# Performance work log

Measured on AMD Instinct MI355X. Metric: run time of the kernel, lower is better.

Reference implementation:

```python
import jax, jax.numpy as jnp
import numpy as np

N_NODES = 10000
N_EDGES = 160000
HIDDEN = 128
NGAUSS = 100
NF = 64
N_CONV = 2


def setup_inputs() -> dict:
    key = jax.random.key(0)
    ks = jax.random.split(key, 10)
    h = jax.random.normal(ks[0], (N_NODES, HIDDEN), dtype=jnp.float32)
    edge_index = jax.random.randint(ks[1], (2, N_EDGES), 0, N_NODES, dtype=jnp.int64)
    edge_weight = jax.random.uniform(ks[2], (N_EDGES,), dtype=jnp.float32)
    edge_attr = jax.random.normal(ks[3], (N_EDGES, NGAUSS), dtype=jnp.float32)
    data = jnp.zeros((1,), dtype=jnp.float32)
    s = 0.05
    lin0_w = jax.random.normal(ks[4], (HIDDEN, NF), dtype=jnp.float32) * s
    lin0_b = jnp.zeros((NF,), dtype=jnp.float32)
    nn_w1 = jax.random.normal(ks[5], (NGAUSS, HIDDEN), dtype=jnp.float32) * s
    nn_b1 = jnp.zeros((HIDDEN,), dtype=jnp.float32)
    nn_w2 = jax.random.normal(ks[6], (HIDDEN, NF * NF), dtype=jnp.float32) * s
    nn_b2 = jnp.zeros((NF * NF,), dtype=jnp.float32)
    root_w = jax.random.normal(ks[7], (NF, NF), dtype=jnp.float32) * s
    conv_b = jnp.zeros((NF,), dtype=jnp.float32)
    return {"h": h, "edge_index": edge_index, "edge_weight": edge_weight,
            "edge_attr": edge_attr, "data": data,
            "lin0_w": lin0_w, "lin0_b": lin0_b,
            "nn_w1": nn_w1, "nn_b1": nn_b1, "nn_w2": nn_w2, "nn_b2": nn_b2,
            "root_w": root_w, "conv_b": conv_b}


def reference(h, edge_index, edge_weight, edge_attr, data,
              lin0_w, lin0_b, nn_w1, nn_b1, nn_w2, nn_b2, root_w, conv_b):
    # lin0 + relu -> node features x: [N, nf]
    x = jax.nn.relu(h @ lin0_w + lin0_b)

    # edge network: per-edge weight matrix W_e: [E, nf, nf]
    hidden = jax.nn.relu(edge_attr @ nn_w1 + nn_b1)
    W_e = (hidden @ nn_w2 + nn_b2).reshape(N_EDGES, NF, NF)

    src = edge_index[0]  # message source (x_j)
    dst = edge_index[1]  # aggregation target (i)

    # in-degree for mean aggregation (0-degree nodes -> 0 output)
    deg = jax.ops.segment_sum(jnp.ones((N_EDGES,), x.dtype), dst, num_segments=N_NODES)
    inv_deg = (1.0 / jnp.maximum(deg, 1.0))[:, None]  # [N, 1]

    # n_conv applications of the SAME NNConv (shared weights)
    for _ in range(N_CONV):
        msg = jnp.einsum('ei,eio->eo', x[src], W_e)  # gather + per-edge matvec
        agg = jax.ops.segment_sum(msg, dst, num_segments=N_NODES) * inv_deg
        x = agg + x @ root_w + conv_b
    return x
```

## Files before the change

### kernel.cpp

```cpp
#include <hip/hip_runtime.h>

#define N_NODES 10000
#define N_EDGES 160000
#define HID 128
#define NG 100
#define NF 64
#define NIO 4096
#define NJ 8192
#define M_PAD 10240

#define PREP_LIN0 2500
#define PREP_WPT (PREP_LIN0 + 2112)

typedef short bf16x8 __attribute__((ext_vector_type(8)));
typedef float f32x4 __attribute__((ext_vector_type(4)));

__device__ __forceinline__ unsigned short f2b(float f) {
    unsigned int u = __float_as_uint(f);
    u += 0x7fffu + ((u >> 16) & 1u);
    return (unsigned short)(u >> 16);
}
__device__ __forceinline__ float b2f(unsigned short s) { return __uint_as_float((unsigned int)s << 16); }

__device__ __forceinline__ long fidx64(int row, int k) {
    return (long)(row >> 4) * 1024 + (k >> 5) * 512 + ((((k >> 3) & 3) * 16 + (row & 15))) * 8 + (k & 7);
}
__device__ __forceinline__ long fidx128(int row, int k) {
    return (long)(row >> 4) * 2048 + (k >> 5) * 512 + ((((k >> 3) & 3) * 16 + (row & 15))) * 8 + (k & 7);
}

__global__ void hist_kernel(const int* __restrict__ src, const int* __restrict__ dst,
                            float* __restrict__ deg, int* __restrict__ cnt) {
    int e = blockIdx.x * 256 + threadIdx.x;
    if (e < N_EDGES) {
        atomicAdd(&deg[dst[e]], 1.0f);
        atomicAdd(&cnt[src[e]], 1);
    }
}

#define SCAN_C 40
__global__ void scan_kernel(const int* __restrict__ cnt, const float* __restrict__ deg,
                            int* __restrict__ rowptr, float* __restrict__ invd) {
    __shared__ int wsum[4];
    int t = threadIdx.x, wv = t >> 6, l = t & 63;
    int base_i = t * SCAN_C;
    int loc[SCAN_C];
    int sum = 0;
#pragma unroll
    for (int j = 0; j < SCAN_C; ++j) {
        int g = base_i + j;
        int v = (g < N_NODES) ? cnt[g] : 0;
        loc[j] = sum;
        sum += v;
    }
    int incl = sum;
    for (int off = 1; off < 64; off <<= 1) {
        int v = __shfl_up(incl, off);
        if (l >= off) incl += v;
    }
    if (l == 63) wsum[wv] = incl;
    __syncthreads();
    int wbase = 0;
#pragma unroll
    for (int w = 0; w < 4; ++w) wbase += (w < wv) ? wsum[w] : 0;
    int tbase = wbase + incl - sum;
#pragma unroll
    for (int j = 0; j < SCAN_C; ++j) {
        int g = base_i + j;
        if (g <= N_NODES) rowptr[g] = tbase + loc[j];
        if (g < N_NODES) invd[g] = 1.0f / fmaxf(deg[g], 1.0f);
    }
}

__global__ void scatter_kernel(const int* __restrict__ src, const int* __restrict__ dst,
                               const int* __restrict__ rowptr, int* __restrict__ fill,
                               int* __restrict__ rankOf, int* __restrict__ dstp) {
    int e = blockIdx.x * 256 + threadIdx.x;
    if (e < N_EDGES) {
        int s = src[e];
        int r = rowptr[s] + atomicAdd(&fill[s], 1);
        rankOf[e] = r;
        dstp[r] = dst[e];
    }
}

__global__ void prep_kernel(const float* __restrict__ h, const float* __restrict__ lw,
                            const float* __restrict__ lb, const float* __restrict__ b2,
                            float* __restrict__ x, unsigned short* __restrict__ xh,
                            float* __restrict__ xb2,
                            const float* __restrict__ w1, const float* __restrict__ w2,
                            unsigned short* __restrict__ w1h, unsigned short* __restrict__ w2h) {
    int bid = blockIdx.x;
    if (bid < PREP_LIN0) {
        int wv = threadIdx.x >> 6, l = threadIdx.x & 63;
        int n = bid * 4 + wv;
        float h0 = h[n * HID + l];
        float h1 = h[n * HID + 64 + l];
        float acc = lb[l];
#pragma unroll
        for (int i = 0; i < 64; ++i) {
            acc += __shfl(h0, i) * lw[i * NF + l];
            acc += __shfl(h1, i) * lw[(64 + i) * NF + l];
        }
        float v = fmaxf(acc, 0.0f);
        x[n * NF + l] = v;
        xh[fidx64(n, l)] = f2b(v);
        float xb = 0.0f;
#pragma unroll
        for (int i = 0; i < 64; ++i) xb += __shfl(v, i) * b2[i * 64 + l];
        xb2[n * NF + l] = xb;
    } else {
        int id = (bid - PREP_LIN0) * 256 + threadIdx.x;
        if (id < HID * HID) {
            int k = id & 127, c = id >> 7;
            float v = (k < NG) ? w1[k * HID + c] : 0.0f;
            w1h[fidx128(c, k)] = f2b(v);
        } else {
            int id2 = id - HID * HID;
            int i = id2 & 63, j = id2 >> 6;
            int o = j >> 7, k = j & 127;
            w2h[fidx64(j, i)] = f2b(w2[k * NIO + i * 64 + o]);
        }
    }
}

__launch_bounds__(256)
__global__ void hgemm_kernel(const float* __restrict__ ea, const int* __restrict__ rankOf,
                             const unsigned short* __restrict__ w1h,
                             const float* __restrict__ b1, unsigned short* __restrict__ hidp) {
    __shared__ float stg[4][1056];
    const int tid = threadIdx.x, wv = tid >> 6, l = tid & 63;
    const long grow = (long)blockIdx.x * 128;
    const int wr = (wv >> 1) * 64, wc = (wv & 1) * 64;
    const long bpan0 = (wc >> 4);
    const int lc = l & 15, lk = l >> 4;
    const int r8 = l >> 3, cg = l & 7;

    int rks[4][2];
#pragma unroll
    for (int m = 0; m < 4; ++m)
#pragma unroll
        for (int it = 0; it < 2; ++it)
            rks[m][it] = rankOf[grow + wr + m * 16 + it * 8 + r8];

    f32x4 acc[4][4] = {};
#pragma unroll
    for (int ks = 0; ks < 4; ++ks) {
        const int c0 = ks * 32 + lk * 8;
        bf16x8 a[4], b[4];
#pragma unroll
        for (int m = 0; m < 4; ++m) {
            const float* Ar = ea + (grow + wr + m * 16 + lc) * (long)NG;
            f32x4 lo = {0.0f, 0.0f, 0.0f, 0.0f}, hi = {0.0f, 0.0f, 0.0f, 0.0f};
            if (c0 <= 88) {
                lo = *(const f32x4*)(Ar + c0);
                hi = *(const f32x4*)(Ar + c0 + 4);
            } else if (c0 == 96) {
                lo = *(const f32x4*)(Ar + 96);
            }
            bf16x8 t;
            t[0] = f2b(lo[0]); t[1] = f2b(lo[1]); t[2] = f2b(lo[2]); t[3] = f2b(lo[3]);
            t[4] = f2b(hi[0]); t[5] = f2b(hi[1]); t[6] = f2b(hi[2]); t[7] = f2b(hi[3]);
            a[m] = t;
        }
#pragma unroll
        for (int n = 0; n < 4; ++n)
            b[n] = *(const bf16x8*)(w1h + (bpan0 + n) * 2048 + ks * 512 + (long)l * 8);
#pragma unroll
        for (int m = 0; m < 4; ++m)
#pragma unroll
            for (int n = 0; n < 4; ++n)
                acc[m][n] = __builtin_amdgcn_mfma_f32_16x16x32_bf16(a[m], b[n], acc[m][n], 0, 0, 0);
    }

    float* s = stg[wv];
#pragma unroll
    for (int m = 0; m < 4; ++m) {
#pragma unroll
        for (int n = 0; n < 4; ++n)
#pragma unroll
            for (int q = 0; q < 4; ++q)
                s[((l >> 4) * 4 + q) * 66 + n * 16 + (l & 15)] = acc[m][n][q];
#pragma unroll
        for (int it = 0; it < 2; ++it) {
            int row = it * 8 + r8;
            const float* sr = s + row * 66 + cg * 8;
            int colbase = wc + cg * 8;
            unsigned int u[4];
#pragma unroll
            for (int p = 0; p < 4; ++p) {
                float f0 = fmaxf(sr[2 * p] + b1[colbase + 2 * p], 0.0f);
                float f1 = fmaxf(sr[2 * p + 1] + b1[colbase + 2 * p + 1], 0.0f);
                u[p] = ((unsigned int)f2b(f1) << 16) | f2b(f0);
            }
            long Ro = rks[m][it];
            *(uint4*)(hidp + Ro * HID + colbase) = make_uint4(u[0], u[1], u[2], u[3]);
        }
    }
}

__launch_bounds__(256)
__global__ void ygemm_kernel(const unsigned short* __restrict__ xh,
                             const unsigned short* __restrict__ wh,
                             unsigned short* __restrict__ y, int n0) {
    __shared__ float stg[4][1056];
    const int tid = threadIdx.x, wv = tid >> 6, l = tid & 63;
    const int grow = blockIdx.x * 128;
    const int col0base = blockIdx.y * 256;
    const int wr = (wv >> 1) * 64, wc = (wv & 1) * 64;
    const long apan0 = ((n0 + grow + wr) >> 4);
    const int r8 = l >> 3, cg = l & 7;

    bf16x8 a[2][4];
#pragma unroll
    for (int ks = 0; ks < 2; ++ks)
#pragma unroll
        for (int m = 0; m < 4; ++m)
            a[ks][m] = *(const bf16x8*)(xh + (apan0 + m) * 1024 + ks * 512 + (long)l * 8);

    for (int ct = 0; ct < 2; ++ct) {
        const int col0 = col0base + ct * 128;
        const long bpan0 = ((col0 + wc) >> 4);
        f32x4 acc[4][4] = {};
#pragma unroll
        for (int ks = 0; ks < 2; ++ks) {
            bf16x8 b[4];
#pragma unroll
            for (int n = 0; n < 4; ++n)
                b[n] = *(const bf16x8*)(wh + (bpan0 + n) * 1024 + ks * 512 + (long)l * 8);
#pragma unroll
            for (int m = 0; m < 4; ++m)
#pragma unroll
                for (int n = 0; n < 4; ++n)
                    acc[m][n] = __builtin_amdgcn_mfma_f32_16x16x32_bf16(a[ks][m], b[n], acc[m][n], 0, 0, 0);
        }

        float* s = stg[wv];
#pragma unroll
        for (int m = 0; m < 4; ++m) {
#pragma unroll
            for (int n = 0; n < 4; ++n)
#pragma unroll
                for (int q = 0; q < 4; ++q)
                    s[((l >> 4) * 4 + q) * 66 + n * 16 + (l & 15)] = acc[m][n][q];
#pragma unroll
            for (int it = 0; it < 2; ++it) {
                int row = it * 8 + r8;
                const float* sr = s + row * 66 + cg * 8;
                unsigned int u[4];
#pragma unroll
                for (int p = 0; p < 4; ++p)
                    u[p] = ((unsigned int)f2b(sr[2 * p + 1]) << 16) | f2b(sr[2 * p]);
                long R = grow + wr + m * 16 + row;
                *(uint4*)(y + R * NJ + col0 + wc + cg * 8) = make_uint4(u[0], u[1], u[2], u[3]);
            }
        }
    }
}

__global__ void matvec_mfma_kernel(const unsigned short* __restrict__ y,
                                   const unsigned short* __restrict__ hidp,
                                   const int* __restrict__ rowptr, const int* __restrict__ dstp,
                                   const float* __restrict__ xb2, float* __restrict__ agg,
                                   int n0, int n1) {
    int wv = threadIdx.x >> 6, l = threadIdx.x & 63;
    int s = n0 + blockIdx.x * 4 + wv;
    if (s >= n1) return;
    int r0 = rowptr[s], r1 = rowptr[s + 1];
    if (r0 == r1) return;
    int lc = l & 15, lk = l >> 4;

    const unsigned short* Ys = y + (long)(s - n0) * NJ;
    bf16x8 b[4][4];
    float xb2v[4];
#pragma unroll
    for (int og = 0; og < 4; ++og) {
        const unsigned short* Yo = Ys + (og * 16 + lc) * HID + lk * 8;
#pragma unroll
        for (int ks = 0; ks < 4; ++ks) b[og][ks] = *(const bf16x8*)(Yo + ks * 32);
        xb2v[og] = xb2[(long)s * NF + og * 16 + lc];
    }

    for (int mt = r0; mt < r1; mt += 16) {
        const unsigned short* Hs = hidp + (long)(mt + lc) * HID + lk * 8;
        bf16x8 a[4];
#pragma unroll
        for (int ks = 0; ks < 4; ++ks) a[ks] = *(const bf16x8*)(Hs + ks * 32);
        f32x4 acc[4] = {};
#pragma unroll
        for (int og = 0; og < 4; ++og)
#pragma unroll
            for (int ks = 0; ks < 4; ++ks)
                acc[og] = __builtin_amdgcn_mfma_f32_16x16x32_bf16(a[ks], b[og][ks], acc[og], 0, 0, 0);
#pragma unroll
        for (int q = 0; q < 4; ++q) {
            int rank = mt + lk * 4 + q;
            if (rank < r1) {
                long base = (long)dstp[rank] * NF;
#pragma unroll
                for (int og = 0; og < 4; ++og)
                    atomicAdd(&agg[base + og * 16 + lc], acc[og][q] + xb2v[og]);
            }
        }
    }
}

__global__ void combine_kernel(const float* __restrict__ x, float* __restrict__ agg,
                               const float* __restrict__ invd, const float* __restrict__ rw,
                               const float* __restrict__ cb, const float* __restrict__ b2,
                               float* __restrict__ xo, unsigned short* __restrict__ xh,
                               float* __restrict__ xb2) {
    int wv = threadIdx.x >> 6, l = threadIdx.x & 63;
    int n = blockIdx.x * 4 + wv;
    float xv = x[n * NF + l];
    float acc = cb[l];
#pragma unroll
    for (int i = 0; i < 64; ++i) acc += __shfl(xv, i) * rw[i * NF + l];
    float av = agg[n * NF + l];
    agg[n * NF + l] = 0.0f;
    float v = av * invd[n] + acc;
    xo[n * NF + l] = v;
    if (xh) {
        xh[fidx64(n, l)] = f2b(v);
        float xb = 0.0f;
#pragma unroll
        for (int i = 0; i < 64; ++i) xb += __shfl(v, i) * b2[i * 64 + l];
        xb2[n * NF + l] = xb;
    }
}

extern "C" void kernel_launch(void* const* d_in, const int* in_sizes, int n_in,
                              void* d_out, int out_size, void* d_ws, size_t ws_size,
                              hipStream_t stream) {
    const float* h = (const float*)d_in[0];
    const int* ei = (const int*)d_in[1];
    const float* ea = (const float*)d_in[3];
    const float* lin0_w = (const float*)d_in[5];
    const float* lin0_b = (const float*)d_in[6];
    const float* nn_w1 = (const float*)d_in[7];
    const float* nn_b1 = (const float*)d_in[8];
    const float* nn_w2 = (const float*)d_in[9];
    const float* nn_b2 = (const float*)d_in[10];
    const float* root_w = (const float*)d_in[11];
    const float* conv_b = (const float*)d_in[12];
    const int* srcIdx = ei;
    const int* dstIdx = ei + N_EDGES;

    const size_t fixed =
        (size_t)(N_EDGES + 16) * HID * 2 +
        (size_t)NJ * NF * 2 +
        (size_t)HID * HID * 2 +
        (size_t)M_PAD * NF * 2 +
        (size_t)N_NODES * NF * 4 * 4 +
        3 * 40192 +
        (size_t)N_NODES * 4 +
        (size_t)(N_NODES + 1) * 4 +
        (size_t)N_EDGES * 4 * 2 +
        32768;
    int nc = 0, CSn = 0;
    size_t region_bytes = 0;
    for (int c = 2; c <= 16; c *= 2) {
        int csn = (((N_NODES + c - 1) / c) + 127) & ~127;
        size_t rb = (size_t)csn * NJ * 2;
        if (fixed + rb <= ws_size) { nc = c; CSn = csn; region_bytes = rb; break; }
    }
    if (nc == 0) {
        hipMemsetAsync(d_out, 0, (size_t)out_size * 4, stream);
        return;
    }

    char* ws = (char*)d_ws;
    size_t off = 0;
    auto alloc = [&](size_t bytes) {
        char* p = ws + off;
        off += (bytes + 255) & ~(size_t)255;
        return p;
    };
    unsigned short* y = (unsigned short*)alloc(region_bytes);
    unsigned short* hidp = (unsigned short*)alloc((size_t)(N_EDGES + 16) * HID * 2);
    unsigned short* w2h = (unsigned short*)alloc((size_t)NJ * NF * 2);
    unsigned short* w1h = (unsigned short*)alloc((size_t)HID * HID * 2);
    unsigned short* xh = (unsigned short*)alloc((size_t)M_PAD * NF * 2);
    float* xA = (float*)alloc((size_t)N_NODES * NF * 4);
    float* xB = (float*)alloc((size_t)N_NODES * NF * 4);
    float* agg = (float*)alloc((size_t)N_NODES * NF * 4);
    float* xb2 = (float*)alloc((size_t)N_NODES * NF * 4);
    char* degblk = alloc(3 * 40192);
    float* deg = (float*)degblk;
    int* cnt = (int*)(degblk + 40192);
    int* fill = (int*)(degblk + 2 * 40192);
    float* invd = (float*)alloc((size_t)N_NODES * 4);
    int* rowptr = (int*)alloc((size_t)(N_NODES + 1) * 4);
    int* rankOf = (int*)alloc((size_t)N_EDGES * 4);
    int* dstp = (int*)alloc((size_t)N_EDGES * 4);

    hipMemsetAsync(degblk, 0, 3 * 40192, stream);
    hipMemsetAsync(agg, 0, (size_t)N_NODES * NF * 4, stream);
    hist_kernel<<<(N_EDGES + 255) / 256, 256, 0, stream>>>(srcIdx, dstIdx, deg, cnt);
    scan_kernel<<<1, 256, 0, stream>>>(cnt, deg, rowptr, invd);
    scatter_kernel<<<(N_EDGES + 255) / 256, 256, 0, stream>>>(srcIdx, dstIdx, rowptr, fill, rankOf, dstp);
    prep_kernel<<<PREP_WPT, 256, 0, stream>>>(h, lin0_w, lin0_b, nn_b2, xA, xh, xb2,
                                              nn_w1, nn_w2, w1h, w2h);
    hgemm_kernel<<<N_EDGES / 128, 256, 0, stream>>>(ea, rankOf, w1h, nn_b1, hidp);

    for (int conv = 0; conv < 2; ++conv) {
        const float* xin = conv ? xB : xA;
        float* xout = conv ? (float*)d_out : xB;
        unsigned short* mh = conv ? nullptr : xh;

        for (int c = 0; c < nc; ++c) {
            int n0 = c * CSn;
            int n1 = n0 + CSn; if (n1 > N_NODES) n1 = N_NODES;
            if (n0 >= N_NODES) break;
            int gx = (n1 - n0 + 127) / 128;
            ygemm_kernel<<<dim3(gx, NJ / 256), 256, 0, stream>>>(xh, w2h, y, n0);
            matvec_mfma_kernel<<<(n1 - n0 + 3) / 4, 256, 0, stream>>>(y, hidp, rowptr, dstp,
                                                                      xb2, agg, n0, n1);
        }
        combine_kernel<<<N_NODES / 4, 256, 0, stream>>>(xin, agg, invd, root_w, conv_b, nn_b2,
                                                        xout, mh, xb2);
    }
}
```

Before: 333.6 us.

## Overlap ygemm chunks with hgemm and matvec via fused heterogeneous launches

Merges the histogram pass into the prep kernel and folds the two memsets into one by placing the degree block right after agg. When the workspace can hold two y chunks at once, the first chunk's ygemm runs in the same launch as the edge hidden GEMM. The second chunk's ygemm runs in the same launch as the first chunk's matvec, so independent work shares one grid and fewer stalls occur between launches. The cost is a larger y workspace and more complex control flow, with a fallback to the old chunked path when memory is short.

```diff
diff --git a/kernel.cpp b/kernel.cpp
--- a/kernel.cpp
+++ b/kernel.cpp
@@ -9,8 +9,9 @@
 #define NJ 8192
 #define M_PAD 10240
 
-#define PREP_LIN0 2500
-#define PREP_WPT (PREP_LIN0 + 2112)
+#define HP_HIST 625
+#define HP_LIN0 (HP_HIST + 2500)
+#define HP_WPT (HP_LIN0 + 2112)
 
 typedef short bf16x8 __attribute__((ext_vector_type(8)));
 typedef float f32x4 __attribute__((ext_vector_type(4)));
@@ -27,15 +28,6 @@
 }
 __device__ __forceinline__ long fidx128(int row, int k) {
     return (long)(row >> 4) * 2048 + (k >> 5) * 512 + ((((k >> 3) & 3) * 16 + (row & 15))) * 8 + (k & 7);
-}
-
-__global__ void hist_kernel(const int* __restrict__ src, const int* __restrict__ dst,
-                            float* __restrict__ deg, int* __restrict__ cnt) {
-    int e = blockIdx.x * 256 + threadIdx.x;
-    if (e < N_EDGES) {
-        atomicAdd(&deg[dst[e]], 1.0f);
-        atomicAdd(&cnt[src[e]], 1);
-    }
 }
 
 #define SCAN_C 40
@@ -84,16 +76,24 @@
     }
 }
 
-__global__ void prep_kernel(const float* __restrict__ h, const float* __restrict__ lw,
-                            const float* __restrict__ lb, const float* __restrict__ b2,
-                            float* __restrict__ x, unsigned short* __restrict__ xh,
-                            float* __restrict__ xb2,
-                            const float* __restrict__ w1, const float* __restrict__ w2,
-                            unsigned short* __restrict__ w1h, unsigned short* __restrict__ w2h) {
+__global__ void histprep_kernel(const int* __restrict__ src, const int* __restrict__ dst,
+                                float* __restrict__ deg, int* __restrict__ cnt,
+                                const float* __restrict__ h, const float* __restrict__ lw,
+                                const float* __restrict__ lb, const float* __restrict__ b2,
+                                float* __restrict__ x, unsigned short* __restrict__ xh,
+                                float* __restrict__ xb2,
+                                const float* __restrict__ w1, const float* __restrict__ w2,
+                                unsigned short* __restrict__ w1h, unsigned short* __restrict__ w2h) {
     int bid = blockIdx.x;
-    if (bid < PREP_LIN0) {
+    if (bid < HP_HIST) {
+        int e = bid * 256 + threadIdx.x;
+        if (e < N_EDGES) {
+            atomicAdd(&deg[dst[e]], 1.0f);
+            atomicAdd(&cnt[src[e]], 1);
+        }
+    } else if (bid < HP_LIN0) {
         int wv = threadIdx.x >> 6, l = threadIdx.x & 63;
-        int n = bid * 4 + wv;
+        int n = (bid - HP_HIST) * 4 + wv;
         float h0 = h[n * HID + l];
         float h1 = h[n * HID + 64 + l];
         float acc = lb[l];
@@ -110,7 +110,7 @@
         for (int i = 0; i < 64; ++i) xb += __shfl(v, i) * b2[i * 64 + l];
         xb2[n * NF + l] = xb;
     } else {
-        int id = (bid - PREP_LIN0) * 256 + threadIdx.x;
+        int id = (bid - HP_LIN0) * 256 + threadIdx.x;
         if (id < HID * HID) {
             int k = id & 127, c = id >> 7;
             float v = (k < NG) ? w1[k * HID + c] : 0.0f;
@@ -124,13 +124,13 @@
     }
 }
 
-__launch_bounds__(256)
-__global__ void hgemm_kernel(const float* __restrict__ ea, const int* __restrict__ rankOf,
-                             const unsigned short* __restrict__ w1h,
-                             const float* __restrict__ b1, unsigned short* __restrict__ hidp) {
-    __shared__ float stg[4][1056];
+
+__device__ __forceinline__ void hgemm_body(const float* __restrict__ ea, const int* __restrict__ rankOf,
+                                           const unsigned short* __restrict__ w1h,
+                                           const float* __restrict__ b1, unsigned short* __restrict__ hidp,
+                                           int bid, float (*stg)[1056]) {
     const int tid = threadIdx.x, wv = tid >> 6, l = tid & 63;
-    const long grow = (long)blockIdx.x * 128;
+    const long grow = (long)bid * 128;
     const int wr = (wv >> 1) * 64, wc = (wv & 1) * 64;
     const long bpan0 = (wc >> 4);
     const int lc = l & 15, lk = l >> 4;
@@ -199,63 +199,126 @@
     }
 }
 
+__device__ __forceinline__ void ygemm_body(const unsigned short* __restrict__ xh,
+                                           const unsigned short* __restrict__ wh,
+                                           unsigned short* __restrict__ y, int n0,
+                                           int bx, int by, float (*stg)[1056]) {
+    const int tid = threadIdx.x, wv = tid >> 6, l = tid & 63;
+    const int grow = bx * 128;
+    const int col0base = by * 256;
+    const int wr = (wv >> 1) * 64, wc = (wv & 1) * 64;
+    const long apan0 = ((n0 + grow + wr) >> 4);
+    const int r8 = l >> 3, cg = l & 7;
+
+    bf16x8 a[2][4];
+#pragma unroll
+    for (int ks = 0; ks < 2; ++ks)
+#pragma unroll
+        for (int m = 0; m < 4; ++m)
+            a[ks][m] = *(const bf16x8*)(xh + (apan0 + m) * 1024 + ks * 512 + (long)l * 8);
+
+    for (int ct = 0; ct < 2; ++ct) {
+        const int col0 = col0base + ct * 128;
+        const long bpan0 = ((col0 + wc) >> 4);
+        f32x4 acc[4][4] = {};
+#pragma unroll
+        for (int ks = 0; ks < 2; ++ks) {
+            bf16x8 b[4];
+#pragma unroll
+            for (int n = 0; n < 4; ++n)
+                b[n] = *(const bf16x8*)(wh + (bpan0 + n) * 1024 + ks * 512 + (long)l * 8);
+#pragma unroll
+            for (int m = 0; m < 4; ++m)
+#pragma unroll
+                for (int n = 0; n < 4; ++n)
+                    acc[m][n] = __builtin_amdgcn_mfma_f32_16x16x32_bf16(a[ks][m], b[n], acc[m][n], 0, 0, 0);
+        }
+
+        float* s = stg[wv];
+#pragma unroll
+        for (int m = 0; m < 4; ++m) {
+#pragma unroll
+            for (int n = 0; n < 4; ++n)
+#pragma unroll
+                for (int q = 0; q < 4; ++q)
+                    s[((l >> 4) * 4 + q) * 66 + n * 16 + (l & 15)] = acc[m][n][q];
+#pragma unroll
+            for (int it = 0; it < 2; ++it) {
+                int row = it * 8 + r8;
+                const float* sr = s + row * 66 + cg * 8;
+                unsigned int u[4];
+#pragma unroll
+                for (int p = 0; p < 4; ++p)
+                    u[p] = ((unsigned int)f2b(sr[2 * p + 1]) << 16) | f2b(sr[2 * p]);
+                long R = grow + wr + m * 16 + row;
+                *(uint4*)(y + R * NJ + col0 + wc + cg * 8) = make_uint4(u[0], u[1], u[2], u[3]);
+            }
+        }
+    }
+}
+
+__device__ __forceinline__ void matvec_body(const unsigned short* __restrict__ y,
+                                            const unsigned short* __restrict__ hidp,
+                                            const int* __restrict__ rowptr, const int* __restrict__ dstp,
+                                            const float* __restrict__ xb2, float* __restrict__ agg,
+                                            int n0, int n1, int bid) {
+    int wv = threadIdx.x >> 6, l = threadIdx.x & 63;
+    int s = n0 + bid * 4 + wv;
+    if (s >= n1) return;
+    int r0 = rowptr[s], r1 = rowptr[s + 1];
+    if (r0 == r1) return;
+    int lc = l & 15, lk = l >> 4;
+
+    const unsigned short* Ys = y + (long)(s - n0) * NJ;
+    bf16x8 b[4][4];
+    float xb2v[4];
+#pragma unroll
+    for (int og = 0; og < 4; ++og) {
+        const unsigned short* Yo = Ys + (og * 16 + lc) * HID + lk * 8;
+#pragma unroll
+        for (int ks = 0; ks < 4; ++ks) b[og][ks] = *(const bf16x8*)(Yo + ks * 32);
+        xb2v[og] = xb2[(long)s * NF + og * 16 + lc];
+    }
+
+    for (int mt = r0; mt < r1; mt += 16) {
+        const unsigned short* Hs = hidp + (long)(mt + lc) * HID + lk * 8;
+        bf16x8 a[4];
+#pragma unroll
+        for (int ks = 0; ks < 4; ++ks) a[ks] = *(const bf16x8*)(Hs + ks * 32);
+        f32x4 acc[4] = {};
+#pragma unroll
+        for (int og = 0; og < 4; ++og)
+#pragma unroll
+            for (int ks = 0; ks < 4; ++ks)
+                acc[og] = __builtin_amdgcn_mfma_f32_16x16x32_bf16(a[ks], b[og][ks], acc[og], 0, 0, 0);
+#pragma unroll
+        for (int q = 0; q < 4; ++q) {
+            int rank = mt + lk * 4 + q;
+            if (rank < r1) {
+                long base = (long)dstp[rank] * NF;
+#pragma unroll
+                for (int og = 0; og < 4; ++og)
+                    atomicAdd(&agg[base + og * 16 + lc], acc[og][q] + xb2v[og]);
+            }
+        }
+    }
+}
+
+
+__launch_bounds__(256)
+__global__ void hgemm_kernel(const float* __restrict__ ea, const int* __restrict__ rankOf,
+                             const unsigned short* __restrict__ w1h,
+                             const float* __restrict__ b1, unsigned short* __restrict__ hidp) {
+    __shared__ float stg[4][1056];
+    hgemm_body(ea, rankOf, w1h, b1, hidp, blockIdx.x, stg);
+}
+
 __launch_bounds__(256)
 __global__ void ygemm_kernel(const unsigned short* __restrict__ xh,
                              const unsigned short* __restrict__ wh,
                              unsigned short* __restrict__ y, int n0) {
     __shared__ float stg[4][1056];
-    const int tid = threadIdx.x, wv = tid >> 6, l = tid & 63;
-    const int grow = blockIdx.x * 128;
-    const int col0base = blockIdx.y * 256;
-    const int wr = (wv >> 1) * 64, wc = (wv & 1) * 64;
-    const long apan0 = ((n0 + grow + wr) >> 4);
-    const int r8 = l >> 3, cg = l & 7;
-
-    bf16x8 a[2][4];
-#pragma unroll
-    for (int ks = 0; ks < 2; ++ks)
-#pragma unroll
-        for (int m = 0; m < 4; ++m)
-            a[ks][m] = *(const bf16x8*)(xh + (apan0 + m) * 1024 + ks * 512 + (long)l * 8);
-
-    for (int ct = 0; ct < 2; ++ct) {
-        const int col0 = col0base + ct * 128;
-        const long bpan0 = ((col0 + wc) >> 4);
-        f32x4 acc[4][4] = {};
-#pragma unroll
-        for (int ks = 0; ks < 2; ++ks) {
-            bf16x8 b[4];
-#pragma unroll
-            for (int n = 0; n < 4; ++n)
-                b[n] = *(const bf16x8*)(wh + (bpan0 + n) * 1024 + ks * 512 + (long)l * 8);
-#pragma unroll
-            for (int m = 0; m < 4; ++m)
-#pragma unroll
-                for (int n = 0; n < 4; ++n)
-                    acc[m][n] = __builtin_amdgcn_mfma_f32_16x16x32_bf16(a[ks][m], b[n], acc[m][n], 0, 0, 0);
-        }
-
-        float* s = stg[wv];
-#pragma unroll
-        for (int m = 0; m < 4; ++m) {
-#pragma unroll
-            for (int n = 0; n < 4; ++n)
-#pragma unroll
-                for (int q = 0; q < 4; ++q)
-                    s[((l >> 4) * 4 + q) * 66 + n * 16 + (l & 15)] = acc[m][n][q];
-#pragma unroll
-            for (int it = 0; it < 2; ++it) {
-                int row = it * 8 + r8;
-                const float* sr = s + row * 66 + cg * 8;
-                unsigned int u[4];
-#pragma unroll
-                for (int p = 0; p < 4; ++p)
-                    u[p] = ((unsigned int)f2b(sr[2 * p + 1]) << 16) | f2b(sr[2 * p]);
-                long R = grow + wr + m * 16 + row;
-                *(uint4*)(y + R * NJ + col0 + wc + cg * 8) = make_uint4(u[0], u[1], u[2], u[3]);
-            }
-        }
-    }
+    ygemm_body(xh, wh, y, n0, blockIdx.x, blockIdx.y, stg);
 }
 
 __global__ void matvec_mfma_kernel(const unsigned short* __restrict__ y,
@@ -263,45 +326,37 @@
                                    const int* __restrict__ rowptr, const int* __restrict__ dstp,
                                    const float* __restrict__ xb2, float* __restrict__ agg,
                                    int n0, int n1) {
-    int wv = threadIdx.x >> 6, l = threadIdx.x & 63;
-    int s = n0 + blockIdx.x * 4 + wv;
-    if (s >= n1) return;
-    int r0 = rowptr[s], r1 = rowptr[s + 1];
-    if (r0 == r1) return;
-    int lc = l & 15, lk = l >> 4;
-
-    const unsigned short* Ys = y + (long)(s - n0) * NJ;
-    bf16x8 b[4][4];
-    float xb2v[4];
-#pragma unroll
-    for (int og = 0; og < 4; ++og) {
-        const unsigned short* Yo = Ys + (og * 16 + lc) * HID + lk * 8;
-#pragma unroll
-        for (int ks = 0; ks < 4; ++ks) b[og][ks] = *(const bf16x8*)(Yo + ks * 32);
-        xb2v[og] = xb2[(long)s * NF + og * 16 + lc];
-    }
-
-    for (int mt = r0; mt < r1; mt += 16) {
-        const unsigned short* Hs = hidp + (long)(mt + lc) * HID + lk * 8;
-        bf16x8 a[4];
-#pragma unroll
-        for (int ks = 0; ks < 4; ++ks) a[ks] = *(const bf16x8*)(Hs + ks * 32);
-        f32x4 acc[4] = {};
-#pragma unroll
-        for (int og = 0; og < 4; ++og)
-#pragma unroll
-            for (int ks = 0; ks < 4; ++ks)
-                acc[og] = __builtin_amdgcn_mfma_f32_16x16x32_bf16(a[ks], b[og][ks], acc[og], 0, 0, 0);
-#pragma unroll
-        for (int q = 0; q < 4; ++q) {
-            int rank = mt + lk * 4 + q;
-            if (rank < r1) {
-                long base = (long)dstp[rank] * NF;
-#pragma unroll
-                for (int og = 0; og < 4; ++og)
-                    atomicAdd(&agg[base + og * 16 + lc], acc[og][q] + xb2v[og]);
-            }
-        }
+    matvec_body(y, hidp, rowptr, dstp, xb2, agg, n0, n1, blockIdx.x);
+}
+
+__launch_bounds__(256)
+__global__ void hg_yg_kernel(const float* __restrict__ ea, const int* __restrict__ rankOf,
+                             const unsigned short* __restrict__ w1h, const float* __restrict__ b1,
+                             unsigned short* __restrict__ hidp,
+                             const unsigned short* __restrict__ xh, const unsigned short* __restrict__ w2h,
+                             unsigned short* __restrict__ y0, int hgBlocks, int gx) {
+    __shared__ float stg[4][1056];
+    int b = blockIdx.x;
+    if (b < hgBlocks) {
+        hgemm_body(ea, rankOf, w1h, b1, hidp, b, stg);
+    } else {
+        int fb = b - hgBlocks;
+        ygemm_body(xh, w2h, y0, 0, fb % gx, fb / gx, stg);
+    }
+}
+
+__launch_bounds__(256)
+__global__ void mv_yg_kernel(const unsigned short* __restrict__ yR, const unsigned short* __restrict__ hidp,
+                             const int* __restrict__ rowptr, const int* __restrict__ dstp,
+                             const float* __restrict__ xb2, float* __restrict__ agg, int n0M, int n1M,
+                             const unsigned short* __restrict__ xh, const unsigned short* __restrict__ w2h,
+                             unsigned short* __restrict__ yW, int n0Y, int ygBlocks, int gx) {
+    __shared__ float stg[4][1056];
+    int b = blockIdx.x;
+    if (b < ygBlocks) {
+        ygemm_body(xh, w2h, yW, n0Y, b % gx, b / gx, stg);
+    } else {
+        matvec_body(yR, hidp, rowptr, dstp, xb2, agg, n0M, n1M, b - ygBlocks);
     }
 }
 
@@ -357,16 +412,25 @@
         (size_t)(N_NODES + 1) * 4 +
         (size_t)N_EDGES * 4 * 2 +
         32768;
+
+    const int CS0 = (((N_NODES + 1) / 2) + 127) & ~127;
+    const int Y1R = ((N_NODES - CS0 + 127) / 128) * 128;
+    bool overlap = fixed + ((size_t)CS0 + Y1R) * NJ * 2 <= ws_size;
+
     int nc = 0, CSn = 0;
     size_t region_bytes = 0;
-    for (int c = 2; c <= 16; c *= 2) {
-        int csn = (((N_NODES + c - 1) / c) + 127) & ~127;
-        size_t rb = (size_t)csn * NJ * 2;
-        if (fixed + rb <= ws_size) { nc = c; CSn = csn; region_bytes = rb; break; }
-    }
-    if (nc == 0) {
-        hipMemsetAsync(d_out, 0, (size_t)out_size * 4, stream);
-        return;
+    if (overlap) {
+        region_bytes = ((size_t)CS0 + Y1R) * NJ * 2;
+    } else {
+        for (int c = 2; c <= 16; c *= 2) {
+            int csn = (((N_NODES + c - 1) / c) + 127) & ~127;
+            size_t rb = (size_t)csn * NJ * 2;
+            if (fixed + rb <= ws_size) { nc = c; CSn = csn; region_bytes = rb; break; }
+        }
+        if (nc == 0) {
+            hipMemsetAsync(d_out, 0, (size_t)out_size * 4, stream);
+            return;
+        }
     }
 
     char* ws = (char*)d_ws;
@@ -376,7 +440,8 @@
         off += (bytes + 255) & ~(size_t)255;
         return p;
     };
-    unsigned short* y = (unsigned short*)alloc(region_bytes);
+    unsigned short* y0 = (unsigned short*)alloc(region_bytes);
+    unsigned short* y1 = y0 + (size_t)CS0 * NJ;
     unsigned short* hidp = (unsigned short*)alloc((size_t)(N_EDGES + 16) * HID * 2);
     unsigned short* w2h = (unsigned short*)alloc((size_t)NJ * NF * 2);
     unsigned short* w1h = (unsigned short*)alloc((size_t)HID * HID * 2);
@@ -384,40 +449,65 @@
     float* xA = (float*)alloc((size_t)N_NODES * NF * 4);
     float* xB = (float*)alloc((size_t)N_NODES * NF * 4);
     float* agg = (float*)alloc((size_t)N_NODES * NF * 4);
-    float* xb2 = (float*)alloc((size_t)N_NODES * NF * 4);
     char* degblk = alloc(3 * 40192);
     float* deg = (float*)degblk;
     int* cnt = (int*)(degblk + 40192);
     int* fill = (int*)(degblk + 2 * 40192);
+    float* xb2 = (float*)alloc((size_t)N_NODES * NF * 4);
     float* invd = (float*)alloc((size_t)N_NODES * 4);
     int* rowptr = (int*)alloc((size_t)(N_NODES + 1) * 4);
     int* rankOf = (int*)alloc((size_t)N_EDGES * 4);
     int* dstp = (int*)alloc((size_t)N_EDGES * 4);
 
-    hipMemsetAsync(degblk, 0, 3 * 40192, stream);
-    hipMemsetAsync(agg, 0, (size_t)N_NODES * NF * 4, stream);
-    hist_kernel<<<(N_EDGES + 255) / 256, 256, 0, stream>>>(srcIdx, dstIdx, deg, cnt);
+    hipMemsetAsync(agg, 0, (size_t)N_NODES * NF * 4 + 3 * 40192, stream);
+    histprep_kernel<<<HP_WPT, 256, 0, stream>>>(srcIdx, dstIdx, deg, cnt,
+                                                h, lin0_w, lin0_b, nn_b2, xA, xh, xb2,
+                                                nn_w1, nn_w2, w1h, w2h);
     scan_kernel<<<1, 256, 0, stream>>>(cnt, deg, rowptr, invd);
     scatter_kernel<<<(N_EDGES + 255) / 256, 256, 0, stream>>>(srcIdx, dstIdx, rowptr, fill, rankOf, dstp);
-    prep_kernel<<<PREP_WPT, 256, 0, stream>>>(h, lin0_w, lin0_b, nn_b2, xA, xh, xb2,
-                                              nn_w1, nn_w2, w1h, w2h);
-    hgemm_kernel<<<N_EDGES / 128, 256, 0, stream>>>(ea, rankOf, w1h, nn_b1, hidp);
-
-    for (int conv = 0; conv < 2; ++conv) {
-        const float* xin = conv ? xB : xA;
-        float* xout = conv ? (float*)d_out : xB;
-        unsigned short* mh = conv ? nullptr : xh;
-
-        for (int c = 0; c < nc; ++c) {
-            int n0 = c * CSn;
-            int n1 = n0 + CSn; if (n1 > N_NODES) n1 = N_NODES;
-            if (n0 >= N_NODES) break;
-            int gx = (n1 - n0 + 127) / 128;
-            ygemm_kernel<<<dim3(gx, NJ / 256), 256, 0, stream>>>(xh, w2h, y, n0);
-            matvec_mfma_kernel<<<(n1 - n0 + 3) / 4, 256, 0, stream>>>(y, hidp, rowptr, dstp,
-                                                                      xb2, agg, n0, n1);
-        }
-        combine_kernel<<<N_NODES / 4, 256, 0, stream>>>(xin, agg, invd, root_w, conv_b, nn_b2,
-                                                        xout, mh, xb2);
-    }
-}
+
+    if (overlap) {
+        const int HG = N_EDGES / 128;
+        const int gx0 = CS0 / 128;
+        const int gx1 = Y1R / 128;
+        const int yg0 = gx0 * (NJ / 256);
+        const int yg1 = gx1 * (NJ / 256);
+        const int mv0 = (CS0 + 3) / 4;
+        const int mv1 = (N_NODES - CS0 + 3) / 4;
+
+        hg_yg_kernel<<<HG + yg0, 256, 0, stream>>>(ea, rankOf, w1h, nn_b1, hidp,
+                                                   xh, w2h, y0, HG, gx0);
+        for (int conv = 0; conv < 2; ++conv) {
+            const float* xin = conv ? xB : xA;
+            float* xout = conv ? (float*)d_out : xB;
+            unsigned short* mh = conv ? nullptr : xh;
+
+            if (conv == 1)
+                ygemm_kernel<<<dim3(gx0, NJ / 256), 256, 0, stream>>>(xh, w2h, y0, 0);
+            mv_yg_kernel<<<yg1 + mv0, 256, 0, stream>>>(y0, hidp, rowptr, dstp, xb2, agg, 0, CS0,
+                                                        xh, w2h, y1, CS0, yg1, gx1);
+            matvec_mfma_kernel<<<mv1, 256, 0, stream>>>(y1, hidp, rowptr, dstp, xb2, agg,
+                                                        CS0, N_NODES);
+            combine_kernel<<<N_NODES / 4, 256, 0, stream>>>(xin, agg, invd, root_w, conv_b, nn_b2,
+                                                            xout, mh, xb2);
+        }
+    } else {
+        hgemm_kernel<<<N_EDGES / 128, 256, 0, stream>>>(ea, rankOf, w1h, nn_b1, hidp);
+        for (int conv = 0; conv < 2; ++conv) {
+            const float* xin = conv ? xB : xA;
+            float* xout = conv ? (float*)d_out : xB;
+            unsigned short* mh = conv ? nullptr : xh;
+            for (int c = 0; c < nc; ++c) {
+                int n0 = c * CSn;
+                int n1 = n0 + CSn; if (n1 > N_NODES) n1 = N_NODES;
+                if (n0 >= N_NODES) break;
+                int gx = (n1 - n0 + 127) / 128;
+                ygemm_kernel<<<dim3(gx, NJ / 256), 256, 0, stream>>>(xh, w2h, y0, n0);
+                matvec_mfma_kernel<<<(n1 - n0 + 3) / 4, 256, 0, stream>>>(y0, hidp, rowptr, dstp,
+                                                                          xb2, agg, n0, n1);
+            }
+            combine_kernel<<<N_NODES / 4, 256, 0, stream>>>(xin, agg, invd, root_w, conv_b, nn_b2,
+                                                            xout, mh, xb2);
+        }
+    }
+}
```

Result: no change. 336.0 us (+0.7%).
